# Kernel tuning notes

Measured on AMD Instinct MI355X. Metric: run time of the kernel, lower is better.

Reference implementation:

```python
import jax, jax.numpy as jnp
import numpy as np

N, T, F = 4096, 24, 16          # nodes, seq_len, in_features
H = 128                          # temporal_hidden
NH, DO = 4, 32                   # gat num_heads, gat out_features (NH*DO == H)
SEM, PH = 64, 32                 # semantic hidden, predictor hidden
SLOPE = 0.2                      # leaky_relu negative slope
ADJ_P = 0.01                     # adjacency density


def setup_inputs() -> dict:
    key = jax.random.key(0)
    ks = jax.random.split(key, 40)
    f32 = jnp.float32

    def rn(k, shape, s=0.02):
        return jax.random.normal(k, shape, f32) * s

    features = jax.random.normal(ks[0], (N, T, F), f32)
    pos_adj = (jax.random.uniform(ks[1], (N, N)) < ADJ_P).astype(f32)
    neg_adj = (jax.random.uniform(ks[2], (N, N)) < ADJ_P).astype(f32)

    inp = dict(features=features, pos_adj=pos_adj, neg_adj=neg_adj)
    # GRU (torch layout: W_ih [3H,F], W_hh [3H,H], gate order r,z,n)
    inp['gru_Wih'] = rn(ks[3], (3 * H, F), 1.0 / np.sqrt(H))
    inp['gru_Whh'] = rn(ks[4], (3 * H, H), 1.0 / np.sqrt(H))
    inp['gru_bih'] = rn(ks[5], (3 * H,), 1.0 / np.sqrt(H))
    inp['gru_bhh'] = rn(ks[6], (3 * H,), 1.0 / np.sqrt(H))
    # GAT params (linear weights stored [in, out] so we use x @ W)
    i = 7
    for pre in ('pos', 'neg'):
        inp[pre + '_W'] = rn(ks[i], (H, NH * DO)); i += 1
        inp[pre + '_u'] = rn(ks[i], (NH, DO, 1), 1.0); i += 1
        inp[pre + '_v'] = rn(ks[i], (NH, DO, 1), 1.0); i += 1
        inp[pre + '_b'] = rn(ks[i], (1, NH * DO)); i += 1
        inp[pre + '_pW'] = rn(ks[i], (H, NH * DO)); i += 1
        inp[pre + '_pb'] = jnp.zeros((NH * DO,), f32)
    inp['self_W'] = rn(ks[i], (H, H)); i += 1
    inp['self_b'] = jnp.zeros((H,), f32)
    inp['mpos_W'] = rn(ks[i], (NH * DO, H)); i += 1
    inp['mpos_b'] = jnp.zeros((H,), f32)
    inp['mneg_W'] = rn(ks[i], (NH * DO, H)); i += 1
    inp['mneg_b'] = jnp.zeros((H,), f32)
    inp['sem_W1'] = rn(ks[i], (H, SEM)); i += 1
    inp['sem_b1'] = jnp.zeros((SEM,), f32)
    inp['sem_W2'] = rn(ks[i], (SEM, 1)); i += 1
    inp['pred_W1'] = rn(ks[i], (H, PH)); i += 1
    inp['pred_b1'] = jnp.zeros((PH,), f32)
    inp['pred_W2'] = rn(ks[i], (PH, 1)); i += 1
    inp['pred_b2'] = jnp.zeros((1,), f32)
    return inp


def _gru_last(x, Wih, Whh, bih, bhh):
    # x: [N, T, F] -> last hidden state [N, H]
    gi_all = jnp.einsum('ntf,gf->tng', x, Wih) + bih  # precompute input gates [T,N,3H]
    h0 = jnp.zeros((x.shape[0], Whh.shape[1]), x.dtype)

    def step(h, gi):
        gh = h @ Whh.T + bhh
        ir, iz, in_ = jnp.split(gi, 3, axis=-1)
        hr, hz, hn = jnp.split(gh, 3, axis=-1)
        r = jax.nn.sigmoid(ir + hr)
        z = jax.nn.sigmoid(iz + hz)
        n = jnp.tanh(in_ + r * hn)
        return (1.0 - z) * n + z * h, None

    h, _ = jax.lax.scan(step, h0, gi_all)
    return h


def _gat(x, adj, W, u, v, b, pW, pb):
    sup = (x @ W).reshape(-1, NH, DO).transpose(1, 0, 2)     # [NH, N, DO]
    f1 = jnp.matmul(sup, u).reshape(NH, 1, -1)               # [NH, 1, N]
    f2 = jnp.matmul(sup, v).reshape(NH, -1, 1)               # [NH, N, 1]
    w = jax.nn.leaky_relu(f1 + f2, SLOPE)                    # [NH, N, N]
    mw = w * adj                                             # mask
    rs = mw.sum(axis=2, keepdims=True)
    rs = jnp.where(rs == 0, jnp.ones_like(rs), rs)
    attn = mw / rs
    out = jnp.matmul(attn, sup).transpose(1, 0, 2).reshape(-1, NH * DO)
    return out + b + x @ pW + pb                             # bias + residual


def _pairnorm_si(x):
    x = x - x.mean(axis=0)
    rn = jnp.sqrt(1e-6 + (x * x).sum(axis=1, keepdims=True))
    return x / rn


def reference(features, pos_adj, neg_adj,
              gru_Wih, gru_Whh, gru_bih, gru_bhh,
              pos_W, pos_u, pos_v, pos_b, pos_pW, pos_pb,
              neg_W, neg_u, neg_v, neg_b, neg_pW, neg_pb,
              self_W, self_b, mpos_W, mpos_b, mneg_W, mneg_b,
              sem_W1, sem_b1, sem_W2,
              pred_W1, pred_b1, pred_W2, pred_b2):
    support = _gru_last(features, gru_Wih, gru_Whh, gru_bih, gru_bhh)  # [N, H]
    pos_sup = _gat(support, pos_adj, pos_W, pos_u, pos_v, pos_b, pos_pW, pos_pb)
    neg_sup = _gat(support, neg_adj, neg_W, neg_u, neg_v, neg_b, neg_pW, neg_pb)
    self_e = support @ self_W + self_b
    pos_e = pos_sup @ mpos_W + mpos_b
    neg_e = neg_sup @ mneg_W + mneg_b
    emb = jnp.stack([self_e, pos_e, neg_e], axis=1)          # [N, 3, H]
    w = jnp.tanh(emb @ sem_W1 + sem_b1) @ sem_W2             # [N, 3, 1]
    beta = jax.nn.softmax(w, axis=1)
    fused = (beta * emb).sum(axis=1)                          # [N, H]
    fused = _pairnorm_si(fused)
    h = jax.nn.relu(fused @ pred_W1 + pred_b1)               # dropout is eval no-op
    out = jax.nn.sigmoid(h @ pred_W2 + pred_b2).squeeze(-1)  # [N]
    return out
```

## Files before the change

### kernel.cpp

```cpp
#include <hip/hip_runtime.h>


#define NN 4096

typedef unsigned short u16;
typedef unsigned int   u32;
typedef unsigned long long u64;
typedef __attribute__((ext_vector_type(8))) short  short8;
typedef __attribute__((ext_vector_type(4))) float  float4v;

__device__ inline float bf2f(u16 u){ return __uint_as_float(((u32)u)<<16); }
__device__ inline u16 f2bf(float f){
  u32 x = __float_as_uint(f);
  return (u16)((x + 0x7fffu + ((x>>16)&1u))>>16);
}
__device__ inline float ldm(const void* p, int i, int bf){
  return bf ? bf2f(((const u16*)p)[i]) : ((const float*)p)[i];
}
__device__ inline u16 ldm16(const void* p, int i, int bf){
  return bf ? ((const u16*)p)[i] : f2bf(((const float*)p)[i]);
}
__device__ inline float fexp(float x){
  x = fminf(fmaxf(x,-80.f),80.f);
  return __builtin_amdgcn_exp2f(x*1.4426950408889634f);
}
__device__ inline float sigm(float x){
  return __builtin_amdgcn_rcpf(1.f + fexp(-x));
}
__device__ inline float tanhf_(float x){
  float c = fminf(fmaxf(x,-15.f),15.f);
  float e = __builtin_amdgcn_exp2f(c*2.8853900817779268f);
  return (e-1.f)*__builtin_amdgcn_rcpf(e+1.f);
}
__device__ inline float4v mfma16(short8 a, short8 b, float4v c){
  return __builtin_amdgcn_mfma_f32_16x16x32_bf16(a,b,c,0,0,0);
}
__device__ inline int rdbf(const int* __restrict__ mflag){
  int b=0;
  #pragma unroll
  for (int k=0;k<16;k++) b|=mflag[k];
  return b;
}

__global__ __launch_bounds__(256) void k_detect(const u32* __restrict__ adj,
                                                int* __restrict__ mflag,
                                                int* __restrict__ deg)
{
  __shared__ u32 w4[4];
  const int lane=threadIdx.x&63, wv=threadIdx.x>>6;
  int i = (blockIdx.x*256 + threadIdx.x)*4;
  uint4 v = *(const uint4*)(adj + i);
  u32 acc = (v.x | v.y | v.z | v.w) & 0xFFFFu;
  unsigned long long b = __ballot(acc != 0);
  if (lane==0) w4[wv] = (b!=0);
  deg[blockIdx.x*512 + threadIdx.x] = 0;
  deg[blockIdx.x*512 + threadIdx.x + 256] = 0;
  __syncthreads();
  if (threadIdx.x==0) mflag[blockIdx.x] = (w4[0]|w4[1]|w4[2]|w4[3]) ? 1 : 0;
}

__global__ __launch_bounds__(256) void k_imp(
  const int* __restrict__ mflag,
  const void* gWih, const void* gWhh, const void* gbih, const void* gbhh,
  const void* posW, const void* posu, const void* posv, const void* posb,
  const void* pospW, const void* pospb,
  const void* negW, const void* negu, const void* negv, const void* negb,
  const void* negpW, const void* negpb,
  const void* selfW, const void* selfb, const void* mposW, const void* mposb,
  const void* mnegW, const void* mnegb,
  const void* semW1, const void* semb1, const void* semW2,
  const void* predW1, const void* predb1, const void* predW2, const void* predb2,
  u16* __restrict__ Wihb, u16* __restrict__ Whhb,
  u16* __restrict__ WT1,  u16* __restrict__ WT2,
  float* __restrict__ cbrz, float* __restrict__ cbin, float* __restrict__ cbhn,
  float* __restrict__ cuv,  float* __restrict__ cgb,  float* __restrict__ csb,
  float* __restrict__ cw1t, float* __restrict__ cb1,  float* __restrict__ cw2,
  float* __restrict__ cpw1t, float* __restrict__ cpb1, float* __restrict__ cpw2,
  float* __restrict__ cpb2, float* __restrict__ meanacc)
{
  const int bf = rdbf(mflag);
  int i = blockIdx.x*256 + threadIdx.x;
  if (i < 6144){ Wihb[i]=ldm16(gWih,i,bf); return; }  i-=6144;
  if (i < 49152){ Whhb[i]=ldm16(gWhh,i,bf); return; } i-=49152;
  if (i < 81920){
    int m=i>>7,k=i&127,sel=m>>7,ml=m&127;
    const void* s = sel==0?posW: sel==1?pospW: sel==2?negW: sel==3?negpW: selfW;
    WT1[i]=ldm16(s,k*128+ml,bf); return;
  } i-=81920;
  if (i < 32768){
    int m=i>>7,k=i&127;
    const void* s = (m<128)? mposW : mnegW;
    WT2[i]=ldm16(s,k*128+(m&127),bf); return;
  } i-=32768;
  if (i < 256){ cbrz[i]=ldm(gbih,i,bf)+ldm(gbhh,i,bf); return; } i-=256;
  if (i < 128){ cbin[i]=ldm(gbih,256+i,bf); return; } i-=128;
  if (i < 128){ cbhn[i]=ldm(gbhh,256+i,bf); return; } i-=128;
  if (i < 512){
    int s=i>>8, rem=i&255, wh=rem>>7, hd=rem&127;
    const void* p = s? (wh? negv:negu) : (wh? posv:posu);
    cuv[i]=ldm(p,hd,bf); return;
  } i-=512;
  if (i < 256){
    int s=i>>7, d=i&127;
    cgb[i]=ldm(s?negb:posb,d,bf)+ldm(s?negpb:pospb,d,bf); return;
  } i-=256;
  if (i < 384){
    int t=i>>7, d=i&127;
    const void* p = t==0? selfb : t==1? mposb : mnegb;
    csb[i]=ldm(p,d,bf); return;
  } i-=384;
  if (i < 8448){
    int c=i/132, k=i-c*132;
    cw1t[i] = (k<128)? ldm(semW1,k*64+c,bf) : 0.f; return;
  } i-=8448;
  if (i < 64){ cb1[i]=ldm(semb1,i,bf); return; } i-=64;
  if (i < 64){ cw2[i]=ldm(semW2,i,bf); return; } i-=64;
  if (i < 4224){
    int c=i/132, k=i-c*132;
    cpw1t[i] = (k<128)? ldm(predW1,k*32+c,bf) : 0.f; return;
  } i-=4224;
  if (i < 32){ cpb1[i]=ldm(predb1,i,bf); return; } i-=32;
  if (i < 32){ cpw2[i]=ldm(predW2,i,bf); return; } i-=32;
  if (i < 1){ cpb2[i]=ldm(predb2,i,bf); return; } i-=1;
  if (i < 128){ meanacc[i]=0.f; return; }
}

__global__ __launch_bounds__(256) void k_csr(
  const int* __restrict__ mflag,
  const void* posadj, const void* negadj,
  int* __restrict__ deg, u16* __restrict__ idx)
{
  const int bf = rdbf(mflag);
  const int s = blockIdx.y;
  const void* adj = s? negadj : posadj;
  const int lane = threadIdx.x&63;
  const int hr   = blockIdx.x*4 + (threadIdx.x>>6);
  const int row  = hr>>1, half = hr&1;
  u32 mask = 0;
  if (bf){
    const u16* rp = (const u16*)adj + (size_t)row*4096 + half*2048;
    #pragma unroll
    for (int q=0;q<4;q++){
      uint4 v = *(const uint4*)(rp + q*512 + lane*8);
      if (v.x&0xffffu) mask|=1u<<(q*8+0); if (v.x>>16) mask|=1u<<(q*8+1);
      if (v.y&0xffffu) mask|=1u<<(q*8+2); if (v.y>>16) mask|=1u<<(q*8+3);
      if (v.z&0xffffu) mask|=1u<<(q*8+4); if (v.z>>16) mask|=1u<<(q*8+5);
      if (v.w&0xffffu) mask|=1u<<(q*8+6); if (v.w>>16) mask|=1u<<(q*8+7);
    }
  } else {
    const float* rp = (const float*)adj + (size_t)row*4096 + half*2048;
    #pragma unroll
    for (int q=0;q<8;q++){
      uint4 v = *(const uint4*)(rp + q*256 + lane*4);
      if (v.x) mask|=1u<<(q*4+0);
      if (v.y) mask|=1u<<(q*4+1);
      if (v.z) mask|=1u<<(q*4+2);
      if (v.w) mask|=1u<<(q*4+3);
    }
  }
  int cnt = __popc(mask);
  int pre = cnt;
  #pragma unroll
  for (int off=1; off<64; off<<=1){
    int o = __shfl_up(pre, off);
    if (lane>=off) pre += o;
  }
  int tot = __shfl(pre, 63);
  int wbase = 0;
  if (lane==0) wbase = atomicAdd(&deg[s*NN+row], tot);
  wbase = __shfl(wbase, 0);
  int base_p = wbase + pre - cnt;
  u16* out = idx + ((size_t)s*NN + row)*128;
  u32 mm = mask; int k = 0;
  while (mm){
    int b = __ffs(mm)-1; mm &= mm-1;
    int e = bf ? (half*2048 + (b>>3)*512 + lane*8 + (b&7))
               : (half*2048 + (b>>2)*256 + lane*4 + (b&3));
    int p = base_p + k; k++;
    if (p<128) out[p] = (u16)e;
  }
}

__global__ __launch_bounds__(512) void k_gruf(
  const int* __restrict__ mflag, const void* feat,
  const u16* __restrict__ Wihb, const u16* __restrict__ Whhb,
  const float* __restrict__ cbrz, const float* __restrict__ cbin,
  const float* __restrict__ cbhn,
  const u16* __restrict__ WT1, const float* __restrict__ cuv,
  u16* __restrict__ C1b, float* __restrict__ f12)
{
  __shared__ __attribute__((aligned(16))) u16 sh_x[16*392];
  __shared__ __attribute__((aligned(16))) u16 hbuf[2][16*136];
  const int bf = rdbf(mflag);
  const int tid=threadIdx.x, lane=tid&63, wv=tid>>6;
  const int quad=lane>>4, c15=lane&15;
  const int n0=blockIdx.x*16;

  if (bf){
    const u16* f16p=(const u16*)feat;
    for (int i=tid;i<16*384;i+=512){ int n=i/384,e=i-n*384; sh_x[n*392+e]=f16p[(size_t)(n0+n)*384+e]; }
  } else {
    const float* f32p=(const float*)feat;
    for (int i=tid;i<16*384;i+=512){ int n=i/384,e=i-n*384; sh_x[n*392+e]=f2bf(f32p[(size_t)(n0+n)*384+e]); }
  }
  for (int i=tid;i<16*136;i+=512) hbuf[0][i]=0;

  const short8 z8={0,0,0,0,0,0,0,0};
  const float4v z4={0.f,0.f,0.f,0.f};
  short8 bh[3][4], bx3[3];
  #pragma unroll
  for (int g=0;g<3;g++){
    int rowb=(g*8+wv)*16+c15;
    #pragma unroll
    for (int ks=0;ks<4;ks++) bh[g][ks]=*(const short8*)(Whhb+(size_t)rowb*128+ks*32+quad*8);
    bx3[g] = (quad<2)? *(const short8*)(Wihb+(size_t)rowb*16+quad*8) : z8;
  }
  const int j0=wv*16+c15;
  const float brz_r=cbrz[j0], brz_z=cbrz[128+j0];
  const float bin0=cbin[j0],  bhn0=cbhn[j0];
  float hr[4]={0.f,0.f,0.f,0.f};
  __syncthreads();

  for (int t=0;t<24;t++){
    const u16* hb  = hbuf[t&1];
    u16*       hbn = hbuf[(t+1)&1];
    short8 ah[4];
    #pragma unroll
    for (int ks=0;ks<4;ks++) ah[ks]=*(const short8*)(hb + c15*136 + ks*32 + quad*8);
    short8 ax = (quad<2)? *(const short8*)(sh_x + c15*392 + t*16 + quad*8) : z8;
    float4v racc = mfma16(ax,bx3[0],z4);
    float4v zacc = mfma16(ax,bx3[1],z4);
    float4v ni   = mfma16(ax,bx3[2],z4);
    float4v nh   = z4;
    #pragma unroll
    for (int ks=0;ks<4;ks++){
      racc = mfma16(ah[ks],bh[0][ks],racc);
      zacc = mfma16(ah[ks],bh[1][ks],zacc);
      nh   = mfma16(ah[ks],bh[2][ks],nh);
    }
    #pragma unroll
    for (int rr=0;rr<4;rr++){
      const int node = quad*4+rr;
      float r_ = sigm(racc[rr]+brz_r);
      float z_ = sigm(zacc[rr]+brz_z);
      float n_ = tanhf_(ni[rr]+bin0 + r_*(nh[rr]+bhn0));
      float hv = (1.f-z_)*n_ + z_*hr[rr];
      hr[rr]=hv; hbn[node*136+j0]=f2bf(hv);
    }
    __syncthreads();
  }
  short8 a[4];
  #pragma unroll
  for (int ks=0;ks<4;ks++) a[ks]=*(const short8*)(hbuf[0]+c15*136+ks*32+quad*8);
  #pragma unroll
  for (int q=0;q<5;q++){
    int tile=wv*5+q;
    float4v acc={0.f,0.f,0.f,0.f};
    #pragma unroll
    for (int ks=0;ks<4;ks++){
      short8 b=*(const short8*)(WT1+(size_t)(tile*16+c15)*128+ks*32+quad*8);
      acc=mfma16(a[ks],b,acc);
    }
    #pragma unroll
    for (int r=0;r<4;r++)
      C1b[(size_t)(n0+quad*4+r)*640 + tile*16 + c15]=f2bf(acc[r]);
  }
  __syncthreads();
  {
    int q=tid;
    int nl=q&15, h=(q>>4)&3, wsel=(q>>6)&1, s=(q>>7)&1;
    const float* uvp = cuv + s*256 + wsel*128 + h*32;
    const u16*   SL  = C1b + (size_t)(n0+nl)*640 + s*256 + h*32;
    float t=0.f;
    #pragma unroll
    for (int d=0;d<32;d++) t += bf2f(SL[d])*uvp[d];
    f12[s*32768 + wsel*16384 + h*4096 + (n0+nl)] = t;
  }
}

__global__ __launch_bounds__(1024) void k_gat2(
  const u16* __restrict__ C1b, const float* __restrict__ f12,
  const int* __restrict__ deg, const u16* __restrict__ idx,
  const float* __restrict__ cgb, const u16* __restrict__ WT2,
  float* __restrict__ E)
{
  __shared__ u16   nbuf[16][128];
  __shared__ float wbuf[16][4][128];
  __shared__ __attribute__((aligned(16))) u16 sA[16*136];
  const int s=blockIdx.y;
  const int wv=threadIdx.x>>6, lane=threadIdx.x&63;
  const int n0=blockIdx.x*16;
  const int i=n0+wv;
  const int d0=lane, d1=lane+64, h0=lane>>5, h1=2+(lane>>5);
  const float* f1 = f12 + s*32768;
  const float* f2 = f12 + s*32768 + 16384;
  const int dgr = deg[s*NN+i];
  const int dg  = dgr>128 ? 128 : dgr;
  const u16* nb = idx + ((size_t)s*NN+i)*128;
  ((u32*)nbuf[wv])[lane] = ((const u32*)nb)[lane];
  float f2v[4];
  #pragma unroll
  for (int h=0;h<4;h++) f2v[h]=f2[h*4096+i];
  for (int e=lane; e<dg; e+=64){
    int j = nbuf[wv][e];
    #pragma unroll
    for (int h=0;h<4;h++){
      float w = f1[h*4096+j] + f2v[h];
      wbuf[wv][h][e] = w>0.f ? w : 0.2f*w;
    }
  }
  float acc0=0.f,acc1=0.f,rs0=0.f,rs1=0.f;
  #pragma unroll 4
  for (int e=0;e<dg;e++){
    float w0 = wbuf[wv][h0][e];
    float w1 = wbuf[wv][h1][e];
    int j = nbuf[wv][e];
    const u16* SL = C1b + (size_t)j*640 + s*256;
    acc0 += w0*bf2f(SL[d0]); rs0 += w0;
    acc1 += w1*bf2f(SL[d1]); rs1 += w1;
  }
  if (rs0==0.f) rs0=1.f;
  if (rs1==0.f) rs1=1.f;
  const u16* P = C1b + (size_t)i*640 + s*256 + 128;
  sA[wv*136+d0]=f2bf(acc0/rs0 + cgb[s*128+d0] + bf2f(P[d0]));
  sA[wv*136+d1]=f2bf(acc1/rs1 + cgb[s*128+d1] + bf2f(P[d1]));
  __syncthreads();
  if (wv<8){
    const int quad=lane>>4, c15=lane&15;
    short8 a[4];
    #pragma unroll
    for (int ks=0;ks<4;ks++) a[ks]=*(const short8*)(sA+c15*136+ks*32+quad*8);
    const int tile=wv;
    float4v acc={0.f,0.f,0.f,0.f};
    #pragma unroll
    for (int ks=0;ks<4;ks++){
      short8 b=*(const short8*)(WT2+(size_t)(s*128+tile*16+c15)*128+ks*32+quad*8);
      acc=mfma16(a[ks],b,acc);
    }
    #pragma unroll
    for (int r=0;r<4;r++) E[(size_t)(n0+quad*4+r)*256 + s*128 + tile*16 + c15]=acc[r];
  }
}

__global__ __launch_bounds__(256) void k_sem(
  const u16* __restrict__ C1b, const float* __restrict__ E,
  const float* __restrict__ csb, const float* __restrict__ cw1t,
  const float* __restrict__ cb1, const float* __restrict__ cw2,
  float* __restrict__ fused, float* __restrict__ meanacc)
{
  __shared__ float sW1t[64*132];
  __shared__ float sW2[64];
  __shared__ float sb1[64];
  __shared__ float sE[4][3][128];
  __shared__ float redm[4][128];
  const int tid=threadIdx.x, wv=tid>>6, lane=tid&63;
  for (int i=tid;i<8448;i+=256) sW1t[i]=cw1t[i];
  if (tid<64){ sW2[tid]=cw2[tid]; sb1[tid]=cb1[tid]; }
  __syncthreads();
  const float* wcol = sW1t + lane*132;
  float macc0=0.f, macc1=0.f;
  for (int u=0;u<4;u++){
    const int n = blockIdx.x*16 + wv*4 + u;
    for (int d=lane; d<128; d+=64){
      sE[wv][0][d] = bf2f(C1b[(size_t)n*640+512+d]) + csb[d];
      sE[wv][1][d] = E[(size_t)n*256 + d]    + csb[128+d];
      sE[wv][2][d] = E[(size_t)n*256+128+d]  + csb[256+d];
    }
    float sc[3];
    #pragma unroll
    for (int s=0;s<3;s++){
      float t = sb1[lane];
      #pragma unroll
      for (int k=0;k<128;k+=4){
        float4 e4 = *(const float4*)&sE[wv][s][k];
        float4 w4 = *(const float4*)&wcol[k];
        t += e4.x*w4.x + e4.y*w4.y + e4.z*w4.z + e4.w*w4.w;
      }
      t = tanhf_(t);
      float p = t*sW2[lane];
      #pragma unroll
      for (int off=32; off; off>>=1) p += __shfl_xor(p, off);
      sc[s]=p;
    }
    float mx = fmaxf(sc[0], fmaxf(sc[1],sc[2]));
    float e0=fexp(sc[0]-mx), e1=fexp(sc[1]-mx), e2=fexp(sc[2]-mx);
    float inv = 1.f/(e0+e1+e2);
    float b0=e0*inv, b1=e1*inv, b2=e2*inv;
    float f0 = b0*sE[wv][0][lane]    + b1*sE[wv][1][lane]    + b2*sE[wv][2][lane];
    float f1 = b0*sE[wv][0][lane+64] + b1*sE[wv][1][lane+64] + b2*sE[wv][2][lane+64];
    fused[(size_t)n*128+lane]    = f0;
    fused[(size_t)n*128+64+lane] = f1;
    macc0 += f0; macc1 += f1;
  }
  redm[wv][lane]=macc0; redm[wv][lane+64]=macc1;
  __syncthreads();
  if (tid<128)
    atomicAdd(&meanacc[tid], redm[0][tid]+redm[1][tid]+redm[2][tid]+redm[3][tid]);
}

__global__ __launch_bounds__(256) void k_pred(
  const float* __restrict__ fused, const float* __restrict__ meanacc,
  const float* __restrict__ cpw1t, const float* __restrict__ cpb1,
  const float* __restrict__ cpw2, const float* __restrict__ cpb2,
  float* __restrict__ out)
{
  __shared__ float sy[4][128];
  __shared__ float sW1t[32*132];
  __shared__ float sW2[32];
  const int tid=threadIdx.x, wv=tid>>6, lane=tid&63;
  for (int i=tid;i<4224;i+=256) sW1t[i]=cpw1t[i];
  if (tid<32) sW2[tid]=cpw2[tid];
  const int n = blockIdx.x*4 + wv;
  const float inv_n = 1.f/4096.f;
  float x0 = fused[(size_t)n*128+lane]    - meanacc[lane]*inv_n;
  float x1 = fused[(size_t)n*128+64+lane] - meanacc[64+lane]*inv_n;
  float ss = x0*x0 + x1*x1;
  #pragma unroll
  for (int o=32;o;o>>=1) ss += __shfl_xor(ss,o);
  float ir = 1.f/sqrtf(1e-6f + ss);
  sy[wv][lane]=x0*ir; sy[wv][64+lane]=x1*ir;
  __syncthreads();
  const int c = lane&31, half = lane>>5;
  const float* wcol = sW1t + c*132 + half*64;
  const float* yrow = sy[wv] + half*64;
  float h=0.f;
  #pragma unroll
  for (int k=0;k<64;k+=4){
    float4 y4 = *(const float4*)&yrow[k];
    float4 w4 = *(const float4*)&wcol[k];
    h += y4.x*w4.x + y4.y*w4.y + y4.z*w4.z + y4.w*w4.w;
  }
  h += __shfl_xor(h,32);
  h += cpb1[c];
  h = h>0.f? h : 0.f;
  float p = h*sW2[c];
  #pragma unroll
  for (int o=16;o;o>>=1) p += __shfl_xor(p,o);
  if (!lane){
    float z = p + cpb2[0];
    out[n] = __builtin_amdgcn_rcpf(1.f + fexp(-z));
  }
}

extern "C" void kernel_launch(void* const* d_in, const int* in_sizes, int n_in,
                              void* d_out, int out_size, void* d_ws, size_t ws_size,
                              hipStream_t stream)
{
  const void* feat  =d_in[0];
  const void* posadj=d_in[1];
  const void* negadj=d_in[2];
  const void* gWih  =d_in[3];
  const void* gWhh  =d_in[4];
  const void* gbih  =d_in[5];
  const void* gbhh  =d_in[6];
  const void* posW  =d_in[7];
  const void* posu  =d_in[8];
  const void* posv  =d_in[9];
  const void* posb  =d_in[10];
  const void* pospW =d_in[11];
  const void* pospb =d_in[12];
  const void* negW  =d_in[13];
  const void* negu  =d_in[14];
  const void* negv  =d_in[15];
  const void* negb  =d_in[16];
  const void* negpW =d_in[17];
  const void* negpb =d_in[18];
  const void* selfW =d_in[19];
  const void* selfb =d_in[20];
  const void* mposW =d_in[21];
  const void* mposb =d_in[22];
  const void* mnegW =d_in[23];
  const void* mnegb =d_in[24];
  const void* semW1 =d_in[25];
  const void* semb1 =d_in[26];
  const void* semW2 =d_in[27];
  const void* predW1=d_in[28];
  const void* predb1=d_in[29];
  const void* predW2=d_in[30];
  const void* predb2=d_in[31];

  char* wsb=(char*)d_ws; size_t off=0;
  auto alloc=[&](size_t bytes)->void*{ void* p=wsb+off; off+=(bytes+255)&~(size_t)255; return p; };
  int*   mflag=(int*)  alloc(256);
  u16*   Wihb =(u16*)  alloc(6144*2);
  u16*   Whhb =(u16*)  alloc(49152*2);
  u16*   WT1  =(u16*)  alloc(81920*2);
  u16*   WT2  =(u16*)  alloc(32768*2);
  float* cbrz =(float*)alloc(256*4);
  float* cbin =(float*)alloc(128*4);
  float* cbhn =(float*)alloc(128*4);
  float* cuv  =(float*)alloc(512*4);
  float* cgb  =(float*)alloc(256*4);
  float* csb  =(float*)alloc(384*4);
  float* cw1t =(float*)alloc(8448*4);
  float* cb1  =(float*)alloc(64*4);
  float* cw2  =(float*)alloc(64*4);
  float* cpw1t=(float*)alloc(4224*4);
  float* cpb1 =(float*)alloc(32*4);
  float* cpw2 =(float*)alloc(32*4);
  float* cpb2 =(float*)alloc(4);
  u16*   C1b  =(u16*)  alloc((size_t)NN*640*2);
  float* f12  =(float*)alloc((size_t)65536*4);
  int*   deg  =(int*)  alloc((size_t)2*NN*4);
  u16*   nidx =(u16*)  alloc((size_t)2*NN*128*2);
  float* E    =(float*)alloc((size_t)NN*256*4);
  float* fused=(float*)alloc((size_t)NN*128*4);
  float* meanacc=(float*)alloc(128*4);
  (void)ws_size; (void)in_sizes; (void)n_in; (void)out_size;

  k_detect<<<16,          256,0,stream>>>((const u32*)posadj,mflag,deg);
  k_imp   <<<722,         256,0,stream>>>(mflag,gWih,gWhh,gbih,gbhh,
              posW,posu,posv,posb,pospW,pospb,negW,negu,negv,negb,negpW,negpb,
              selfW,selfb,mposW,mposb,mnegW,mnegb,semW1,semb1,semW2,
              predW1,predb1,predW2,predb2,
              Wihb,Whhb,WT1,WT2,cbrz,cbin,cbhn,cuv,cgb,csb,cw1t,cb1,cw2,
              cpw1t,cpb1,cpw2,cpb2,meanacc);
  k_csr   <<<dim3(2048,2),256,0,stream>>>(mflag,posadj,negadj,deg,nidx);
  k_gruf  <<<NN/16,       512,0,stream>>>(mflag,feat,Wihb,Whhb,cbrz,cbin,cbhn,
                                          WT1,cuv,C1b,f12);
  k_gat2  <<<dim3(256,2),1024,0,stream>>>(C1b,f12,deg,nidx,cgb,WT2,E);
  k_sem   <<<NN/16,       256,0,stream>>>(C1b,E,csb,cw1t,cb1,cw2,fused,meanacc);
  k_pred  <<<NN/4,        256,0,stream>>>(fused,meanacc,cpw1t,cpb1,cpw2,cpb2,(float*)d_out);
}
```

Measured before the change: 293.9 us.

## Fuse CSR neighbor-list construction into the GAT aggregation kernel

Removes the separate CSR kernel, which wrote degree counts and neighbor indices to global memory using atomics. Each wave in the GAT kernel now scans its own full adjacency row, computes a prefix scan over lane masks, and writes neighbor indices directly into shared memory. This saves a kernel launch, the global round trip for deg/idx, the atomics and the deg zeroing. In exchange, the dense adjacency read runs inside the GAT kernel with less parallelism per row (one wave per full row instead of two), which could lengthen that kernel.

```diff
diff --git a/kernel.cpp b/kernel.cpp
--- a/kernel.cpp
+++ b/kernel.cpp
@@ -43,8 +43,7 @@
 }
 
 __global__ __launch_bounds__(256) void k_detect(const u32* __restrict__ adj,
-                                                int* __restrict__ mflag,
-                                                int* __restrict__ deg)
+                                                int* __restrict__ mflag)
 {
   __shared__ u32 w4[4];
   const int lane=threadIdx.x&63, wv=threadIdx.x>>6;
@@ -53,8 +52,6 @@
   u32 acc = (v.x | v.y | v.z | v.w) & 0xFFFFu;
   unsigned long long b = __ballot(acc != 0);
   if (lane==0) w4[wv] = (b!=0);
-  deg[blockIdx.x*512 + threadIdx.x] = 0;
-  deg[blockIdx.x*512 + threadIdx.x + 256] = 0;
   __syncthreads();
   if (threadIdx.x==0) mflag[blockIdx.x] = (w4[0]|w4[1]|w4[2]|w4[3]) ? 1 : 0;
 }
@@ -125,62 +122,6 @@
   if (i < 128){ meanacc[i]=0.f; return; }
 }
 
-__global__ __launch_bounds__(256) void k_csr(
-  const int* __restrict__ mflag,
-  const void* posadj, const void* negadj,
-  int* __restrict__ deg, u16* __restrict__ idx)
-{
-  const int bf = rdbf(mflag);
-  const int s = blockIdx.y;
-  const void* adj = s? negadj : posadj;
-  const int lane = threadIdx.x&63;
-  const int hr   = blockIdx.x*4 + (threadIdx.x>>6);
-  const int row  = hr>>1, half = hr&1;
-  u32 mask = 0;
-  if (bf){
-    const u16* rp = (const u16*)adj + (size_t)row*4096 + half*2048;
-    #pragma unroll
-    for (int q=0;q<4;q++){
-      uint4 v = *(const uint4*)(rp + q*512 + lane*8);
-      if (v.x&0xffffu) mask|=1u<<(q*8+0); if (v.x>>16) mask|=1u<<(q*8+1);
-      if (v.y&0xffffu) mask|=1u<<(q*8+2); if (v.y>>16) mask|=1u<<(q*8+3);
-      if (v.z&0xffffu) mask|=1u<<(q*8+4); if (v.z>>16) mask|=1u<<(q*8+5);
-      if (v.w&0xffffu) mask|=1u<<(q*8+6); if (v.w>>16) mask|=1u<<(q*8+7);
-    }
-  } else {
-    const float* rp = (const float*)adj + (size_t)row*4096 + half*2048;
-    #pragma unroll
-    for (int q=0;q<8;q++){
-      uint4 v = *(const uint4*)(rp + q*256 + lane*4);
-      if (v.x) mask|=1u<<(q*4+0);
-      if (v.y) mask|=1u<<(q*4+1);
-      if (v.z) mask|=1u<<(q*4+2);
-      if (v.w) mask|=1u<<(q*4+3);
-    }
-  }
-  int cnt = __popc(mask);
-  int pre = cnt;
-  #pragma unroll
-  for (int off=1; off<64; off<<=1){
-    int o = __shfl_up(pre, off);
-    if (lane>=off) pre += o;
-  }
-  int tot = __shfl(pre, 63);
-  int wbase = 0;
-  if (lane==0) wbase = atomicAdd(&deg[s*NN+row], tot);
-  wbase = __shfl(wbase, 0);
-  int base_p = wbase + pre - cnt;
-  u16* out = idx + ((size_t)s*NN + row)*128;
-  u32 mm = mask; int k = 0;
-  while (mm){
-    int b = __ffs(mm)-1; mm &= mm-1;
-    int e = bf ? (half*2048 + (b>>3)*512 + lane*8 + (b&7))
-               : (half*2048 + (b>>2)*256 + lane*4 + (b&3));
-    int p = base_p + k; k++;
-    if (p<128) out[p] = (u16)e;
-  }
-}
-
 __global__ __launch_bounds__(512) void k_gruf(
   const int* __restrict__ mflag, const void* feat,
   const u16* __restrict__ Wihb, const u16* __restrict__ Whhb,
@@ -278,26 +219,69 @@
   }
 }
 
-__global__ __launch_bounds__(1024) void k_gat2(
+__global__ __launch_bounds__(1024) void k_gat3(
+  const int* __restrict__ mflag,
+  const void* posadj, const void* negadj,
   const u16* __restrict__ C1b, const float* __restrict__ f12,
-  const int* __restrict__ deg, const u16* __restrict__ idx,
   const float* __restrict__ cgb, const u16* __restrict__ WT2,
   float* __restrict__ E)
 {
   __shared__ u16   nbuf[16][128];
   __shared__ float wbuf[16][4][128];
   __shared__ __attribute__((aligned(16))) u16 sA[16*136];
+  const int bf = rdbf(mflag);
   const int s=blockIdx.y;
+  const void* adj = s? negadj : posadj;
   const int wv=threadIdx.x>>6, lane=threadIdx.x&63;
   const int n0=blockIdx.x*16;
   const int i=n0+wv;
-  const int d0=lane, d1=lane+64, h0=lane>>5, h1=2+(lane>>5);
+
+  u64 mask=0;
+  if (bf){
+    const u16* rp = (const u16*)adj + (size_t)i*4096;
+    #pragma unroll
+    for (int it=0; it<8; it++){
+      const uint4 vv = *(const uint4*)(rp + it*512 + lane*8);
+      u32 w[4]={vv.x,vv.y,vv.z,vv.w};
+      #pragma unroll
+      for (int q=0;q<4;q++){
+        if (w[q]&0xffffu) mask |= 1ull<<(it*8+2*q);
+        if (w[q]>>16)     mask |= 1ull<<(it*8+2*q+1);
+      }
+    }
+  } else {
+    const float* rp = (const float*)adj + (size_t)i*4096;
+    #pragma unroll
+    for (int it=0; it<16; it++){
+      const uint4 vv = *(const uint4*)(rp + it*256 + lane*4);
+      if (vv.x) mask |= 1ull<<(it*4+0);
+      if (vv.y) mask |= 1ull<<(it*4+1);
+      if (vv.z) mask |= 1ull<<(it*4+2);
+      if (vv.w) mask |= 1ull<<(it*4+3);
+    }
+  }
+  int cnt=__popcll(mask);
+  int pre=cnt;
+  #pragma unroll
+  for (int off=1; off<64; off<<=1){
+    int o=__shfl_up(pre,off);
+    if (lane>=off) pre+=o;
+  }
+  int base_p = pre-cnt;
+  int total = __shfl(pre,63);
+  const int dg = total>128 ? 128 : total;
+  u64 mm=mask; int k=0;
+  while (mm){
+    int b=__ffsll(mm)-1; mm&=mm-1;
+    int e = bf ? ((b>>3)*512 + lane*8 + (b&7))
+               : ((b>>2)*256 + lane*4 + (b&3));
+    int p=base_p+k; k++;
+    if (p<128) nbuf[wv][p]=(u16)e;
+  }
+
   const float* f1 = f12 + s*32768;
   const float* f2 = f12 + s*32768 + 16384;
-  const int dgr = deg[s*NN+i];
-  const int dg  = dgr>128 ? 128 : dgr;
-  const u16* nb = idx + ((size_t)s*NN+i)*128;
-  ((u32*)nbuf[wv])[lane] = ((const u32*)nb)[lane];
+  const int d0=lane, d1=lane+64, h0=lane>>5, h1=2+(lane>>5);
   float f2v[4];
   #pragma unroll
   for (int h=0;h<4;h++) f2v[h]=f2[h*4096+i];
@@ -309,6 +293,7 @@
       wbuf[wv][h][e] = w>0.f ? w : 0.2f*w;
     }
   }
+
   float acc0=0.f,acc1=0.f,rs0=0.f,rs1=0.f;
   #pragma unroll 4
   for (int e=0;e<dg;e++){
@@ -501,24 +486,21 @@
   float* cpb2 =(float*)alloc(4);
   u16*   C1b  =(u16*)  alloc((size_t)NN*640*2);
   float* f12  =(float*)alloc((size_t)65536*4);
-  int*   deg  =(int*)  alloc((size_t)2*NN*4);
-  u16*   nidx =(u16*)  alloc((size_t)2*NN*128*2);
   float* E    =(float*)alloc((size_t)NN*256*4);
   float* fused=(float*)alloc((size_t)NN*128*4);
   float* meanacc=(float*)alloc(128*4);
   (void)ws_size; (void)in_sizes; (void)n_in; (void)out_size;
 
-  k_detect<<<16,          256,0,stream>>>((const u32*)posadj,mflag,deg);
+  k_detect<<<16,          256,0,stream>>>((const u32*)posadj,mflag);
   k_imp   <<<722,         256,0,stream>>>(mflag,gWih,gWhh,gbih,gbhh,
               posW,posu,posv,posb,pospW,pospb,negW,negu,negv,negb,negpW,negpb,
               selfW,selfb,mposW,mposb,mnegW,mnegb,semW1,semb1,semW2,
               predW1,predb1,predW2,predb2,
               Wihb,Whhb,WT1,WT2,cbrz,cbin,cbhn,cuv,cgb,csb,cw1t,cb1,cw2,
               cpw1t,cpb1,cpw2,cpb2,meanacc);
-  k_csr   <<<dim3(2048,2),256,0,stream>>>(mflag,posadj,negadj,deg,nidx);
   k_gruf  <<<NN/16,       512,0,stream>>>(mflag,feat,Wihb,Whhb,cbrz,cbin,cbhn,
                                           WT1,cuv,C1b,f12);
-  k_gat2  <<<dim3(256,2),1024,0,stream>>>(C1b,f12,deg,nidx,cgb,WT2,E);
+  k_gat3  <<<dim3(256,2),1024,0,stream>>>(mflag,posadj,negadj,C1b,f12,cgb,WT2,E);
   k_sem   <<<NN/16,       256,0,stream>>>(C1b,E,csb,cw1t,cb1,cw2,fused,meanacc);
   k_pred  <<<NN/4,        256,0,stream>>>(fused,meanacc,cpw1t,cpb1,cpw2,cpb2,(float*)d_out);
 }
```

Result: faster. 287.3 us (-2.2%).
